# Kernel tuning notes

Measured on AMD Instinct MI355X. Metric: run time of the kernel, lower is better.

## Reference

```python
import jax, jax.numpy as jnp
import numpy as np

H = 2  # attention heads (n_heads)


def _time_enc(t, tw, tb):
    # TGN TimeEncode: cos(t * w + b); t [...,] -> [..., T]
    return jnp.cos(t[..., None] * tw + tb)


def _level0(nodes, node_features, memory_tab):
    # memory[src] + node_features[src]
    return memory_tab[nodes] + node_features[nodes]


def _aggregate(l, src_feat, src_te, neigh, ete, efeat, mask,
               Wq, bq, Wk, bk, Wv, bv, Wo, bo, fc1_w, fc1_b, fc2_w, fc2_b):
    # Temporal graph attention (TGN TemporalAttentionLayer) with padding mask.
    N, K, _ = neigh.shape
    Dq = Wq.shape[-1]
    dh = Dq // H
    q_in = jnp.concatenate([src_feat[:, None, :], src_te], axis=-1)   # [N,1,Dq]
    k_in = jnp.concatenate([neigh, ete, efeat], axis=-1)              # [N,K,Dk]
    q = (q_in @ Wq[l] + bq[l]).reshape(N, 1, H, dh)
    k = (k_in @ Wk[l] + bk[l]).reshape(N, K, H, dh)
    v = (k_in @ Wv[l] + bv[l]).reshape(N, K, H, dh)
    scores = jnp.einsum('nqhd,nkhd->nhqk', q, k) / jnp.sqrt(jnp.asarray(dh, q.dtype))
    all_masked = mask.all(axis=-1)                                    # [N]
    # TGN trick: un-mask column 0 for fully-masked rows, zero output later
    eff_mask = mask & ~(all_masked[:, None] & (jnp.arange(K) == 0))
    scores = jnp.where(eff_mask[:, None, None, :], -1e9, scores)
    attn = jax.nn.softmax(scores, axis=-1)
    o = jnp.einsum('nhqk,nkhd->nqhd', attn, v).reshape(N, Dq)
    o = o @ Wo[l] + bo[l]
    o = jnp.where(all_masked[:, None], 0.0, o)
    # MergeLayer: fc2(relu(fc1(cat[attn_out, src_feat])))
    h = jax.nn.relu(jnp.concatenate([o, src_feat], axis=-1) @ fc1_w[l] + fc1_b[l])
    return h @ fc2_w[l] + fc2_b[l]


def setup_inputs() -> dict:
    key = jax.random.key(0)
    ks = jax.random.split(key, 24)
    B, K, Nn, Ne, D, T = 2048, 20, 1_000_000, 1_000_000, 128, 128
    Dq, Dk = D + T, D + T + D
    inp = {}
    inp['node_features'] = jax.random.normal(ks[0], (Nn, D), jnp.float32) * 0.1
    inp['edge_feat_table'] = jax.random.normal(ks[1], (Ne, D), jnp.float32) * 0.1
    inp['memory_tab'] = jax.random.normal(ks[2], (Nn, D), jnp.float32) * 0.1
    inp['timestamps'] = jax.random.uniform(ks[3], (B,), jnp.float32) * 100.0
    inp['etimes_src'] = jax.random.uniform(ks[4], (B, K), jnp.float32) * 100.0
    inp['etimes_nbr'] = jax.random.uniform(ks[5], (B * K, K), jnp.float32) * 100.0
    inp['tw'] = jax.random.normal(ks[6], (T,), jnp.float32)
    inp['tb'] = jax.random.normal(ks[7], (T,), jnp.float32)
    inp['Wq'] = jax.random.normal(ks[8], (2, Dq, Dq), jnp.float32) / np.sqrt(Dq)
    inp['bq'] = jnp.zeros((2, Dq), jnp.float32)
    inp['Wk'] = jax.random.normal(ks[9], (2, Dk, Dq), jnp.float32) / np.sqrt(Dk)
    inp['bk'] = jnp.zeros((2, Dq), jnp.float32)
    inp['Wv'] = jax.random.normal(ks[10], (2, Dk, Dq), jnp.float32) / np.sqrt(Dk)
    inp['bv'] = jnp.zeros((2, Dq), jnp.float32)
    inp['Wo'] = jax.random.normal(ks[11], (2, Dq, Dq), jnp.float32) / np.sqrt(Dq)
    inp['bo'] = jnp.zeros((2, Dq), jnp.float32)
    inp['fc1_w'] = jax.random.normal(ks[12], (2, Dq + D, D), jnp.float32) / np.sqrt(Dq + D)
    inp['fc1_b'] = jnp.zeros((2, D), jnp.float32)
    inp['fc2_w'] = jax.random.normal(ks[13], (2, D, D), jnp.float32) / np.sqrt(D)
    inp['fc2_b'] = jnp.zeros((2, D), jnp.float32)
    inp['source_nodes'] = jax.random.randint(ks[14], (B,), 0, Nn)
    inp['nbrs_src'] = jax.random.randint(ks[15], (B, K), 0, Nn)
    inp['eidx_src'] = jax.random.randint(ks[16], (B, K), 0, Ne)
    inp['nbrs_nbr'] = jax.random.randint(ks[17], (B * K, K), 0, Nn)
    inp['eidx_nbr'] = jax.random.randint(ks[18], (B * K, K), 0, Ne)
    return inp


def reference(node_features, edge_feat_table, memory_tab, timestamps,
              etimes_src, etimes_nbr, tw, tb,
              Wq, bq, Wk, bk, Wv, bv, Wo, bo, fc1_w, fc1_b, fc2_w, fc2_b,
              source_nodes, nbrs_src, eidx_src, nbrs_nbr, eidx_nbr):
    B, K = nbrs_src.shape
    D = node_features.shape[-1]
    params = (Wq, bq, Wk, bk, Wv, bv, Wo, bo, fc1_w, fc1_b, fc2_w, fc2_b)

    def layer1(nodes, ts, nbrs, eidx, etimes):
        # one temporal-attention hop (n_layers == 1 recursion level)
        src = _level0(nodes, node_features, memory_tab)                 # [N,D]
        neigh = _level0(nbrs.reshape(-1), node_features, memory_tab).reshape(*nbrs.shape, D)
        ete = _time_enc(ts[:, None] - etimes, tw, tb)                   # [N,K,T]
        src_te = _time_enc(jnp.zeros((nodes.shape[0], 1), ts.dtype), tw, tb)
        efeat = edge_feat_table[eidx]                                   # [N,K,De]
        mask = nbrs == 0
        return _aggregate(0, src, src_te, neigh, ete, efeat, mask, *params)

    # layer-1 embedding of sources (recursion uses same temporal neighbors)
    src_conv = layer1(source_nodes, timestamps, nbrs_src, eidx_src, etimes_src)  # [B,D]
    # layer-1 embedding of the sources' neighbors
    ts_rep = jnp.repeat(timestamps, K)                                  # [B*K]
    neigh_emb = layer1(nbrs_src.reshape(-1), ts_rep, nbrs_nbr, eidx_nbr, etimes_nbr)
    neigh_emb = neigh_emb.reshape(B, K, D)
    # layer-2 aggregation over the sources' neighbors
    ete = _time_enc(timestamps[:, None] - etimes_src, tw, tb)           # [B,K,T]
    src_te = _time_enc(jnp.zeros((B, 1), timestamps.dtype), tw, tb)
    efeat = edge_feat_table[eidx_src]
    mask = nbrs_src == 0
    return _aggregate(1, src_conv, src_te, neigh_emb, ete, efeat, mask, *params)
```

## Files before the change

### kernel.cpp

```cpp
#include <hip/hip_runtime.h>
#include <hip/hip_bf16.h>

#define NB   2048
#define KN   20
#define DF   128
#define DQ   256
#define DKI  384
#define NR1  43008
#define SCALE 0.08838834764831845f

typedef short s16x8 __attribute__((ext_vector_type(8)));
typedef short s16x4 __attribute__((ext_vector_type(4)));
typedef float f32x4 __attribute__((ext_vector_type(4)));

__device__ __hip_bfloat16 g_S   [(size_t)NR1*256];
__device__ __hip_bfloat16 g_QKH [(size_t)NR1*768];
__device__ __hip_bfloat16 g_CTX [(size_t)NR1*768];
__device__ __hip_bfloat16 g_Ob  [(size_t)NR1*256];
__device__ __hip_bfloat16 g_FC1A[(size_t)NR1*384];
__device__ __hip_bfloat16 g_Hb  [(size_t)NR1*128];
__device__ float          g_out1[(size_t)NR1*DF];
__device__ float          g_Wqk [2*256*768];
__device__ float          g_bqk [2*768];
__device__ unsigned char  g_allm[NR1];
__device__ __hip_bfloat16 g_Bqk[2*196608];
__device__ __hip_bfloat16 g_Bv [2*196608];
__device__ __hip_bfloat16 g_Bo [2*65536];
__device__ __hip_bfloat16 g_B1 [2*49152];
__device__ __hip_bfloat16 g_B2 [2*16384];

__device__ __forceinline__ short f2bf(float v) {
  union { __hip_bfloat16 h; short s; } u; u.h = __float2bfloat16(v); return u.s;
}
__device__ __forceinline__ float bf2f(__hip_bfloat16 h) {
  union { __hip_bfloat16 h2[2]; unsigned u; float f; } x;
  x.u = 0; x.h2[1] = h; return x.f;
}
__device__ __forceinline__ s16x4 pack4(float x, float y, float z, float w) {
  s16x4 o; o[0]=f2bf(x); o[1]=f2bf(y); o[2]=f2bf(z); o[3]=f2bf(w); return o;
}

__global__ __launch_bounds__(256)
void k_wqk(const float* __restrict__ Wq, const float* __restrict__ Wk,
           const float* __restrict__ bq) {
  int idx = blockIdx.x*256 + threadIdx.x;
  int L = idx / 196608, rem = idx % 196608;
  int n = rem >> 8, co = rem & 255;
  int h = n / 384, i = n - h*384;
  const float* wqp = Wq + (size_t)L*DQ*DQ  + (size_t)co*DQ + h*128;
  const float* wkp = Wk + (size_t)L*DKI*DQ + (size_t)i*DQ  + h*128;
  float acc = 0.f;
  #pragma unroll 4
  for (int c = 0; c < 128; ++c) acc += wqp[c]*wkp[c];
  g_Wqk[(size_t)(L*256 + co)*768 + n] = acc;
  if (co == 0) {
    const float* bqp = bq + L*DQ + h*128;
    float b = 0.f;
    for (int c = 0; c < 128; ++c) b += bqp[c]*wkp[c];
    g_bqk[L*768 + n] = b;
  }
}

__global__ __launch_bounds__(256)
void k_btile(const float* __restrict__ src, int ldsrc, int K, int N,
             __hip_bfloat16* __restrict__ dst, int blkdiag) {
  int slot = blockIdx.x*256 + threadIdx.x;
  if (slot >= (K*N)/8) return;
  int cl = slot & 15, t = slot >> 4;
  int kgn = K >> 3;
  int kg = t % kgn, nt = t / kgn;
  int n = nt*16 + cl;
  s16x8 o;
  #pragma unroll
  for (int e = 0; e < 8; ++e) {
    int k = kg*8 + e; float v;
    if (blkdiag) { int hk = k / 384; v = (hk == (n >> 7)) ? src[(size_t)(k - hk*384)*ldsrc + n] : 0.f; }
    else v = src[(size_t)k*ldsrc + n];
    o[e] = f2bf(v);
  }
  *(s16x8*)(dst + (size_t)slot*8) = o;
}

template<int L>
__global__ __launch_bounds__(256)
void k_prep(const float* __restrict__ nf, const float* __restrict__ mem,
            const float* __restrict__ tb,
            const int* __restrict__ srcn, const int* __restrict__ nbs) {
  const int tid = threadIdx.x;
  const int rl = tid >> 5, q = tid & 31, d0 = q*4;
  const int r = blockIdx.x*8 + rl;
  float ax, ay, az, aw;
  if (L == 0) {
    int node = (r < NB) ? srcn[r] : nbs[r - NB];
    float4 x = *(const float4*)(mem + (size_t)node*DF + d0);
    float4 y = *(const float4*)(nf  + (size_t)node*DF + d0);
    ax=x.x+y.x; ay=x.y+y.y; az=x.z+y.z; aw=x.w+y.w;
  } else {
    float4 x = *(const float4*)(g_out1 + (size_t)r*DF + d0);
    ax=x.x; ay=x.y; az=x.z; aw=x.w;
  }
  *(s16x4*)(g_S + (size_t)r*256 + d0) = pack4(ax, ay, az, aw);
  *(s16x4*)(g_S + (size_t)r*256 + 128 + d0) =
      pack4(cosf(tb[d0]), cosf(tb[d0+1]), cosf(tb[d0+2]), cosf(tb[d0+3]));
  *(s16x4*)(g_FC1A + (size_t)r*384 + 256 + d0) = pack4(ax, ay, az, aw);
}

template<int L>
__global__ __launch_bounds__(256)
void k_edge(const float* __restrict__ nf, const float* __restrict__ ef,
            const float* __restrict__ mem, const float* __restrict__ tsv,
            const float* __restrict__ ets, const float* __restrict__ etn,
            const float* __restrict__ tw,  const float* __restrict__ tb,
            const int* __restrict__ nbs, const int* __restrict__ eis,
            const int* __restrict__ nbn, const int* __restrict__ ein,
            const __hip_bfloat16* __restrict__ QKH,
            __hip_bfloat16* __restrict__ CTX)
{
  const int r = blockIdx.x, tid = threadIdx.x;
  const int lane = tid & 63, w = tid >> 6;

  __shared__ int   nd[KN], ei[KN];
  __shared__ float dts[KN];
  __shared__ float s_sh[2][KN];
  __shared__ float aw_sh[2][KN];
  __shared__ float ctxp[4][768];
  __shared__ unsigned mbits_sh;

  int raw_ = 1;
  if (tid < KN) {
    int nd_, ei_; float dt_;
    if (L == 0) {
      if (r < NB) { raw_ = nbs[r*KN+tid]; nd_ = raw_; ei_ = eis[r*KN+tid]; dt_ = tsv[r] - ets[r*KN+tid]; }
      else { int mm = (r-NB)*KN + tid; raw_ = nbn[mm]; nd_ = raw_; ei_ = ein[mm]; dt_ = tsv[(r-NB)/KN] - etn[mm]; }
    } else {
      raw_ = nbs[r*KN+tid]; nd_ = NB + r*KN + tid; ei_ = eis[r*KN+tid]; dt_ = tsv[r] - ets[r*KN+tid];
    }
    nd[tid] = nd_; ei[tid] = ei_; dts[tid] = dt_;
  }
  if (tid < 64) {
    unsigned long long bal = __ballot(tid < KN && raw_ == 0);
    if (tid == 0) {
      unsigned mb = (unsigned)(bal & 0xFFFFFull);
      mbits_sh = mb;
      g_allm[r] = (mb == 0xFFFFFu) ? 1 : 0;
    }
  }

  float q0[6], q1[6];
  #pragma unroll
  for (int j = 0; j < 6; ++j) {
    q0[j] = bf2f(QKH[(size_t)r*768 +       j*64 + lane]);
    q1[j] = bf2f(QKH[(size_t)r*768 + 384 + j*64 + lane]);
  }
  float twr0 = tw[lane],      twr1 = tw[64 + lane];
  float tbr0 = tb[lane],      tbr1 = tb[64 + lane];
  __syncthreads();

  float ve[5][6];
  #pragma unroll
  for (int e = 0; e < 5; ++e) {
    const int m = w*5 + e;
    const int nd_ = nd[m], ei_ = ei[m];
    const float dt_ = dts[m];
    float v0, v1;
    if (L == 0) {
      v0 = mem[(size_t)nd_*DF +      lane] + nf[(size_t)nd_*DF +      lane];
      v1 = mem[(size_t)nd_*DF + 64 + lane] + nf[(size_t)nd_*DF + 64 + lane];
    } else {
      v0 = g_out1[(size_t)nd_*DF +      lane];
      v1 = g_out1[(size_t)nd_*DF + 64 + lane];
    }
    float v2 = __cosf(dt_*twr0 + tbr0);
    float v3 = __cosf(dt_*twr1 + tbr1);
    float v4 = ef[(size_t)ei_*DF +      lane];
    float v5 = ef[(size_t)ei_*DF + 64 + lane];
    ve[e][0]=v0; ve[e][1]=v1; ve[e][2]=v2; ve[e][3]=v3; ve[e][4]=v4; ve[e][5]=v5;
    float p0 = v0*q0[0] + v1*q0[1] + v2*q0[2] + v3*q0[3] + v4*q0[4] + v5*q0[5];
    float p1 = v0*q1[0] + v1*q1[1] + v2*q1[2] + v3*q1[3] + v4*q1[4] + v5*q1[5];
    #pragma unroll
    for (int off = 1; off < 64; off <<= 1) {
      p0 += __shfl_xor(p0, off);
      p1 += __shfl_xor(p1, off);
    }
    if (lane == 0) { s_sh[0][m] = p0; s_sh[1][m] = p1; }
  }
  __syncthreads();

  if (tid < 64) {
    const int h = tid >> 5, mm = tid & 31;
    const unsigned mb = mbits_sh;
    float sc;
    if (mm < KN) sc = ((mb >> mm) & 1u) ? -1e9f : s_sh[h][mm] * SCALE;
    else         sc = -3.0e38f;
    float mx = sc;
    #pragma unroll
    for (int off = 1; off < 32; off <<= 1) mx = fmaxf(mx, __shfl_xor(mx, off));
    float ev = (mm < KN) ? __expf(sc - mx) : 0.f;
    float sum = ev;
    #pragma unroll
    for (int off = 1; off < 32; off <<= 1) sum += __shfl_xor(sum, off);
    if (mm < KN) aw_sh[h][mm] = ev / sum;
  }
  __syncthreads();

  {
    float c0[6] = {0,0,0,0,0,0}, c1[6] = {0,0,0,0,0,0};
    #pragma unroll
    for (int e = 0; e < 5; ++e) {
      const int m = w*5 + e;
      const float a0 = aw_sh[0][m], a1 = aw_sh[1][m];
      #pragma unroll
      for (int j = 0; j < 6; ++j) {
        c0[j] += a0 * ve[e][j];
        c1[j] += a1 * ve[e][j];
      }
    }
    #pragma unroll
    for (int j = 0; j < 6; ++j) {
      ctxp[w][      j*64 + lane] = c0[j];
      ctxp[w][384 + j*64 + lane] = c1[j];
    }
  }
  __syncthreads();

  #pragma unroll
  for (int it = 0; it < 3; ++it) {
    int o = it*256 + tid;
    float s = ctxp[0][o] + ctxp[1][o] + ctxp[2][o] + ctxp[3][o];
    CTX[(size_t)r*768 + o] = __float2bfloat16(s);
  }
}

template<int KT, bool F32OUT, bool RELU, bool MASK>
__global__ __launch_bounds__(256, 2)
void k_gemm(const __hip_bfloat16* __restrict__ A, int lda,
            const __hip_bfloat16* __restrict__ B, int kgtot, int nblk,
            void* __restrict__ Cout, int ldc,
            const float* __restrict__ bias,
            const unsigned char* __restrict__ mask)
{
  __shared__ __hip_bfloat16 As[2][128*40];
  __shared__ __hip_bfloat16 Bs[2][128*32];
  const int tid  = threadIdx.x;
  const int lane = tid & 63, wid = tid >> 6;
  const int wm = wid >> 1, wn = wid & 1;
  const int rl = lane & 15, kgs = lane >> 4;
  const int bm = blockIdx.x / nblk, bn = blockIdx.x % nblk;

  f32x4 acc[4][4];
  #pragma unroll
  for (int i = 0; i < 4; ++i)
    #pragma unroll
    for (int j = 0; j < 4; ++j) acc[i][j] = (f32x4){0.f,0.f,0.f,0.f};

  #define STAGE(T, BUF) {                                                      \
    _Pragma("unroll")                                                          \
    for (int i_ = 0; i_ < 2; ++i_) {                                           \
      int row_ = i_*64 + (tid >> 2), kc_ = (tid & 3)*8;                        \
      s16x8 v_ = *(const s16x8*)(A + (size_t)(bm*128 + row_)*lda + (T)*32 + kc_); \
      *(s16x8*)(&As[BUF][row_*40 + kc_]) = v_;                                 \
    }                                                                          \
    _Pragma("unroll")                                                          \
    for (int i_ = 0; i_ < 2; ++i_) {                                           \
      int slot_ = i_*256 + tid;                                                \
      int nt_ = slot_ >> 6, kg_ = (slot_ >> 4) & 3, cl_ = slot_ & 15;          \
      s16x8 w_ = *(const s16x8*)(B + ((size_t)(bn*8 + nt_)*kgtot + (T)*4 + kg_)*128 + cl_*8); \
      *(s16x8*)(&Bs[BUF][slot_*8]) = w_;                                       \
    } }

  STAGE(0, 0);
  __syncthreads();
  int buf = 0;
  for (int t = 0; t < KT; ++t) {
    if (t < KT-1) STAGE(t+1, buf ^ 1);
    s16x8 af[4], bfm[4];
    #pragma unroll
    for (int mtl = 0; mtl < 4; ++mtl)
      af[mtl] = *(const s16x8*)(&As[buf][(wm*64 + mtl*16 + rl)*40 + kgs*8]);
    #pragma unroll
    for (int ntl = 0; ntl < 4; ++ntl)
      bfm[ntl] = *(const s16x8*)(&Bs[buf][((wn*4 + ntl)*4 + kgs)*128 + rl*8]);
    #pragma unroll
    for (int mtl = 0; mtl < 4; ++mtl)
      #pragma unroll
      for (int ntl = 0; ntl < 4; ++ntl)
        acc[mtl][ntl] = __builtin_amdgcn_mfma_f32_16x16x32_bf16(af[mtl], bfm[ntl], acc[mtl][ntl], 0, 0, 0);
    __syncthreads();
    buf ^= 1;
  }
  #undef STAGE

  #pragma unroll
  for (int mtl = 0; mtl < 4; ++mtl) {
    #pragma unroll
    for (int ntl = 0; ntl < 4; ++ntl) {
      int gcol = bn*128 + wn*64 + ntl*16 + rl;
      float bb = bias ? bias[gcol] : 0.f;
      #pragma unroll
      for (int rg = 0; rg < 4; ++rg) {
        int grow = bm*128 + wm*64 + mtl*16 + kgs*4 + rg;
        float v = acc[mtl][ntl][rg] + bb;
        if (RELU) v = fmaxf(v, 0.f);
        if (MASK) { if (mask[grow]) v = 0.f; }
        if (F32OUT) ((float*)Cout)[(size_t)grow*ldc + gcol] = v;
        else ((__hip_bfloat16*)Cout)[(size_t)grow*ldc + gcol] = __float2bfloat16(v);
      }
    }
  }
}

extern "C" void kernel_launch(void* const* d_in, const int* in_sizes, int n_in,
                              void* d_out, int out_size, void* d_ws, size_t ws_size,
                              hipStream_t stream) {
  (void)in_sizes; (void)n_in; (void)out_size; (void)ws_size; (void)d_ws;
  const float* nf   = (const float*)d_in[0];
  const float* ef   = (const float*)d_in[1];
  const float* mem  = (const float*)d_in[2];
  const float* tsv  = (const float*)d_in[3];
  const float* ets  = (const float*)d_in[4];
  const float* etn  = (const float*)d_in[5];
  const float* tw   = (const float*)d_in[6];
  const float* tb   = (const float*)d_in[7];
  const float* Wq   = (const float*)d_in[8];
  const float* bq   = (const float*)d_in[9];
  const float* Wk   = (const float*)d_in[10];
  const float* bv   = (const float*)d_in[13];
  const float* Wv   = (const float*)d_in[12];
  const float* Wo   = (const float*)d_in[14];
  const float* bo   = (const float*)d_in[15];
  const float* f1w  = (const float*)d_in[16];
  const float* f1b  = (const float*)d_in[17];
  const float* f2w  = (const float*)d_in[18];
  const float* f2b  = (const float*)d_in[19];
  const int* srcn   = (const int*)d_in[20];
  const int* nbs    = (const int*)d_in[21];
  const int* eis    = (const int*)d_in[22];
  const int* nbn    = (const int*)d_in[23];
  const int* ein    = (const int*)d_in[24];
  float* out = (float*)d_out;

  __hip_bfloat16 *S, *QKH, *CTX, *Ob, *FC1A, *Hb, *Bqk, *Bv, *Bo, *B1, *B2;
  float *Wqkf, *bqkf, *out1f;
  unsigned char* allm;
  hipGetSymbolAddress((void**)&S,    HIP_SYMBOL(g_S));
  hipGetSymbolAddress((void**)&QKH,  HIP_SYMBOL(g_QKH));
  hipGetSymbolAddress((void**)&CTX,  HIP_SYMBOL(g_CTX));
  hipGetSymbolAddress((void**)&Ob,   HIP_SYMBOL(g_Ob));
  hipGetSymbolAddress((void**)&FC1A, HIP_SYMBOL(g_FC1A));
  hipGetSymbolAddress((void**)&Hb,   HIP_SYMBOL(g_Hb));
  hipGetSymbolAddress((void**)&Bqk,  HIP_SYMBOL(g_Bqk));
  hipGetSymbolAddress((void**)&Bv,   HIP_SYMBOL(g_Bv));
  hipGetSymbolAddress((void**)&Bo,   HIP_SYMBOL(g_Bo));
  hipGetSymbolAddress((void**)&B1,   HIP_SYMBOL(g_B1));
  hipGetSymbolAddress((void**)&B2,   HIP_SYMBOL(g_B2));
  hipGetSymbolAddress((void**)&Wqkf, HIP_SYMBOL(g_Wqk));
  hipGetSymbolAddress((void**)&bqkf, HIP_SYMBOL(g_bqk));
  hipGetSymbolAddress((void**)&out1f,HIP_SYMBOL(g_out1));
  hipGetSymbolAddress((void**)&allm, HIP_SYMBOL(g_allm));

  hipLaunchKernelGGL(k_wqk, dim3(1536), dim3(256), 0, stream, Wq, Wk, bq);
  for (int L = 0; L < 2; ++L) {
    hipLaunchKernelGGL(k_btile, dim3(96),  dim3(256), 0, stream, Wqkf + (size_t)L*256*768, 768, 256, 768, Bqk + (size_t)L*196608, 0);
    hipLaunchKernelGGL(k_btile, dim3(96),  dim3(256), 0, stream, Wv + (size_t)L*DKI*DQ,    256, 768, 256, Bv  + (size_t)L*196608, 1);
    hipLaunchKernelGGL(k_btile, dim3(32),  dim3(256), 0, stream, Wo + (size_t)L*DQ*DQ,     256, 256, 256, Bo  + (size_t)L*65536,  0);
    hipLaunchKernelGGL(k_btile, dim3(24),  dim3(256), 0, stream, f1w + (size_t)L*384*128,  128, 384, 128, B1  + (size_t)L*49152,  0);
    hipLaunchKernelGGL(k_btile, dim3(8),   dim3(256), 0, stream, f2w + (size_t)L*128*128,  128, 128, 128, B2  + (size_t)L*16384,  0);
  }

  {
    const int R = NR1, BMg = R/128;
    hipLaunchKernelGGL((k_prep<0>), dim3(R/8), dim3(256), 0, stream, nf, mem, tb, srcn, nbs);
    hipLaunchKernelGGL((k_gemm<8,false,false,false>), dim3(BMg*6), dim3(256), 0, stream,
        S, 256, Bqk, 32, 6, QKH, 768, bqkf, (const unsigned char*)nullptr);
    hipLaunchKernelGGL((k_edge<0>), dim3(R), dim3(256), 0, stream,
        nf, ef, mem, tsv, ets, etn, tw, tb, nbs, eis, nbn, ein, QKH, CTX);
    hipLaunchKernelGGL((k_gemm<24,false,false,false>), dim3(BMg*2), dim3(256), 0, stream,
        CTX, 768, Bv, 96, 2, Ob, 256, bv, (const unsigned char*)nullptr);
    hipLaunchKernelGGL((k_gemm<8,false,false,true>), dim3(BMg*2), dim3(256), 0, stream,
        Ob, 256, Bo, 32, 2, FC1A, 384, bo, allm);
    hipLaunchKernelGGL((k_gemm<12,false,true,false>), dim3(BMg), dim3(256), 0, stream,
        FC1A, 384, B1, 48, 1, Hb, 128, f1b, (const unsigned char*)nullptr);
    hipLaunchKernelGGL((k_gemm<4,true,false,false>), dim3(BMg), dim3(256), 0, stream,
        Hb, 128, B2, 16, 1, out1f, 128, f2b, (const unsigned char*)nullptr);
  }
  {
    const int R = NB, BMg = R/128;
    hipLaunchKernelGGL((k_prep<1>), dim3(R/8), dim3(256), 0, stream, nf, mem, tb, srcn, nbs);
    hipLaunchKernelGGL((k_gemm<8,false,false,false>), dim3(BMg*6), dim3(256), 0, stream,
        S, 256, Bqk + 196608, 32, 6, QKH, 768, bqkf + 768, (const unsigned char*)nullptr);
    hipLaunchKernelGGL((k_edge<1>), dim3(R), dim3(256), 0, stream,
        nf, ef, mem, tsv, ets, etn, tw, tb, nbs, eis, nbn, ein, QKH, CTX);
    hipLaunchKernelGGL((k_gemm<24,false,false,false>), dim3(BMg*2), dim3(256), 0, stream,
        CTX, 768, Bv + 196608, 96, 2, Ob, 256, bv + 256, (const unsigned char*)nullptr);
    hipLaunchKernelGGL((k_gemm<8,false,false,true>), dim3(BMg*2), dim3(256), 0, stream,
        Ob, 256, Bo + 65536, 32, 2, FC1A, 384, bo + 256, allm);
    hipLaunchKernelGGL((k_gemm<12,false,true,false>), dim3(BMg), dim3(256), 0, stream,
        FC1A, 384, B1 + 49152, 48, 1, Hb, 128, f1b + 128, (const unsigned char*)nullptr);
    hipLaunchKernelGGL((k_gemm<4,true,false,false>), dim3(BMg), dim3(256), 0, stream,
        Hb, 128, B2 + 16384, 16, 1, out, 128, f2b + 128, (const unsigned char*)nullptr);
  }
}
```

Before: 635.2 us.

## Split V projection per head and vectorize edge gathers with float2 loads

The block-diagonal V weight, which was padded with zeros to K=768, is replaced by two per-head GEMMs with K=384 each. This halves the MACs and the B-tile traffic of the context projection, at the cost of an extra launch. In the edge kernel, each lane now loads two adjacent elements with float2/packed-bf16 loads, and all gathers are issued before any compute to raise memory-level parallelism. k_edge also gets a launch-bounds occupancy hint, which may limit registers and cause spills.

After: 611.2 us. 1.04x faster.

```diff
diff --git a/kernel.cpp b/kernel.cpp
--- a/kernel.cpp
+++ b/kernel.cpp
@@ -24,7 +24,7 @@
 __device__ float          g_bqk [2*768];
 __device__ unsigned char  g_allm[NR1];
 __device__ __hip_bfloat16 g_Bqk[2*196608];
-__device__ __hip_bfloat16 g_Bv [2*196608];
+__device__ __hip_bfloat16 g_Bv [4*49152];
 __device__ __hip_bfloat16 g_Bo [2*65536];
 __device__ __hip_bfloat16 g_B1 [2*49152];
 __device__ __hip_bfloat16 g_B2 [2*16384];
@@ -32,9 +32,11 @@
 __device__ __forceinline__ short f2bf(float v) {
   union { __hip_bfloat16 h; short s; } u; u.h = __float2bfloat16(v); return u.s;
 }
-__device__ __forceinline__ float bf2f(__hip_bfloat16 h) {
-  union { __hip_bfloat16 h2[2]; unsigned u; float f; } x;
-  x.u = 0; x.h2[1] = h; return x.f;
+__device__ __forceinline__ float2 bfpair(unsigned u) {
+  union { unsigned u2; float f; } a, b;
+  a.u2 = u << 16;
+  b.u2 = u & 0xFFFF0000u;
+  float2 r; r.x = a.f; r.y = b.f; return r;
 }
 __device__ __forceinline__ s16x4 pack4(float x, float y, float z, float w) {
   s16x4 o; o[0]=f2bf(x); o[1]=f2bf(y); o[2]=f2bf(z); o[3]=f2bf(w); return o;
@@ -63,7 +65,7 @@
 
 __global__ __launch_bounds__(256)
 void k_btile(const float* __restrict__ src, int ldsrc, int K, int N,
-             __hip_bfloat16* __restrict__ dst, int blkdiag) {
+             __hip_bfloat16* __restrict__ dst) {
   int slot = blockIdx.x*256 + threadIdx.x;
   if (slot >= (K*N)/8) return;
   int cl = slot & 15, t = slot >> 4;
@@ -72,12 +74,7 @@
   int n = nt*16 + cl;
   s16x8 o;
   #pragma unroll
-  for (int e = 0; e < 8; ++e) {
-    int k = kg*8 + e; float v;
-    if (blkdiag) { int hk = k / 384; v = (hk == (n >> 7)) ? src[(size_t)(k - hk*384)*ldsrc + n] : 0.f; }
-    else v = src[(size_t)k*ldsrc + n];
-    o[e] = f2bf(v);
-  }
+  for (int e = 0; e < 8; ++e) o[e] = f2bf(src[(size_t)(kg*8 + e)*ldsrc + n]);
   *(s16x8*)(dst + (size_t)slot*8) = o;
 }
 
@@ -106,7 +103,7 @@
 }
 
 template<int L>
-__global__ __launch_bounds__(256)
+__global__ __launch_bounds__(256, 6)
 void k_edge(const float* __restrict__ nf, const float* __restrict__ ef,
             const float* __restrict__ mem, const float* __restrict__ tsv,
             const float* __restrict__ ets, const float* __restrict__ etn,
@@ -146,43 +143,54 @@
     }
   }
 
-  float q0[6], q1[6];
-  #pragma unroll
-  for (int j = 0; j < 6; ++j) {
-    q0[j] = bf2f(QKH[(size_t)r*768 +       j*64 + lane]);
-    q1[j] = bf2f(QKH[(size_t)r*768 + 384 + j*64 + lane]);
-  }
-  float twr0 = tw[lane],      twr1 = tw[64 + lane];
-  float tbr0 = tb[lane],      tbr1 = tb[64 + lane];
+  const __hip_bfloat16* Qr = QKH + (size_t)r*768;
+  float2 q0[3], q1[3];
+  #pragma unroll
+  for (int seg = 0; seg < 3; ++seg) {
+    q0[seg] = bfpair(*(const unsigned*)(Qr +       seg*128 + 2*lane));
+    q1[seg] = bfpair(*(const unsigned*)(Qr + 384 + seg*128 + 2*lane));
+  }
+  float2 twr = *(const float2*)(tw + 2*lane);
+  float2 tbr = *(const float2*)(tb + 2*lane);
   __syncthreads();
 
-  float ve[5][6];
+  int   nds[5], eir[5]; float dtr[5];
   #pragma unroll
   for (int e = 0; e < 5; ++e) {
-    const int m = w*5 + e;
-    const int nd_ = nd[m], ei_ = ei[m];
-    const float dt_ = dts[m];
-    float v0, v1;
+    int m = w*5 + e;
+    nds[e] = nd[m]; eir[e] = ei[m]; dtr[e] = dts[m];
+  }
+  float2 vm[5], vf[5], vef[5];
+  #pragma unroll
+  for (int e = 0; e < 5; ++e) {
     if (L == 0) {
-      v0 = mem[(size_t)nd_*DF +      lane] + nf[(size_t)nd_*DF +      lane];
-      v1 = mem[(size_t)nd_*DF + 64 + lane] + nf[(size_t)nd_*DF + 64 + lane];
+      vm[e] = *(const float2*)(mem + (size_t)nds[e]*DF + 2*lane);
+      vf[e] = *(const float2*)(nf  + (size_t)nds[e]*DF + 2*lane);
     } else {
-      v0 = g_out1[(size_t)nd_*DF +      lane];
-      v1 = g_out1[(size_t)nd_*DF + 64 + lane];
-    }
-    float v2 = __cosf(dt_*twr0 + tbr0);
-    float v3 = __cosf(dt_*twr1 + tbr1);
-    float v4 = ef[(size_t)ei_*DF +      lane];
-    float v5 = ef[(size_t)ei_*DF + 64 + lane];
-    ve[e][0]=v0; ve[e][1]=v1; ve[e][2]=v2; ve[e][3]=v3; ve[e][4]=v4; ve[e][5]=v5;
-    float p0 = v0*q0[0] + v1*q0[1] + v2*q0[2] + v3*q0[3] + v4*q0[4] + v5*q0[5];
-    float p1 = v0*q1[0] + v1*q1[1] + v2*q1[2] + v3*q1[3] + v4*q1[4] + v5*q1[5];
+      vm[e] = *(const float2*)(g_out1 + (size_t)nds[e]*DF + 2*lane);
+    }
+    vef[e] = *(const float2*)(ef + (size_t)eir[e]*DF + 2*lane);
+  }
+
+  float2 vn[5], vt[5];
+  #pragma unroll
+  for (int e = 0; e < 5; ++e) {
+    if (L == 0) { vn[e].x = vm[e].x + vf[e].x; vn[e].y = vm[e].y + vf[e].y; }
+    else        vn[e] = vm[e];
+    vt[e].x = __cosf(dtr[e]*twr.x + tbr.x);
+    vt[e].y = __cosf(dtr[e]*twr.y + tbr.y);
+    float p0 = vn[e].x*q0[0].x + vn[e].y*q0[0].y
+             + vt[e].x*q0[1].x + vt[e].y*q0[1].y
+             + vef[e].x*q0[2].x + vef[e].y*q0[2].y;
+    float p1 = vn[e].x*q1[0].x + vn[e].y*q1[0].y
+             + vt[e].x*q1[1].x + vt[e].y*q1[1].y
+             + vef[e].x*q1[2].x + vef[e].y*q1[2].y;
     #pragma unroll
     for (int off = 1; off < 64; off <<= 1) {
       p0 += __shfl_xor(p0, off);
       p1 += __shfl_xor(p1, off);
     }
-    if (lane == 0) { s_sh[0][m] = p0; s_sh[1][m] = p1; }
+    if (lane == 0) { s_sh[0][w*5+e] = p0; s_sh[1][w*5+e] = p1; }
   }
   __syncthreads();
 
@@ -204,22 +212,25 @@
   __syncthreads();
 
   {
-    float c0[6] = {0,0,0,0,0,0}, c1[6] = {0,0,0,0,0,0};
+    float2 c0n = {0,0}, c0t = {0,0}, c0e = {0,0};
+    float2 c1n = {0,0}, c1t = {0,0}, c1e = {0,0};
     #pragma unroll
     for (int e = 0; e < 5; ++e) {
       const int m = w*5 + e;
       const float a0 = aw_sh[0][m], a1 = aw_sh[1][m];
-      #pragma unroll
-      for (int j = 0; j < 6; ++j) {
-        c0[j] += a0 * ve[e][j];
-        c1[j] += a1 * ve[e][j];
-      }
-    }
-    #pragma unroll
-    for (int j = 0; j < 6; ++j) {
-      ctxp[w][      j*64 + lane] = c0[j];
-      ctxp[w][384 + j*64 + lane] = c1[j];
-    }
+      c0n.x += a0*vn[e].x;  c0n.y += a0*vn[e].y;
+      c0t.x += a0*vt[e].x;  c0t.y += a0*vt[e].y;
+      c0e.x += a0*vef[e].x; c0e.y += a0*vef[e].y;
+      c1n.x += a1*vn[e].x;  c1n.y += a1*vn[e].y;
+      c1t.x += a1*vt[e].x;  c1t.y += a1*vt[e].y;
+      c1e.x += a1*vef[e].x; c1e.y += a1*vef[e].y;
+    }
+    *(float2*)&ctxp[w][      2*lane] = c0n;
+    *(float2*)&ctxp[w][128 + 2*lane] = c0t;
+    *(float2*)&ctxp[w][256 + 2*lane] = c0e;
+    *(float2*)&ctxp[w][384 + 2*lane] = c1n;
+    *(float2*)&ctxp[w][512 + 2*lane] = c1t;
+    *(float2*)&ctxp[w][640 + 2*lane] = c1e;
   }
   __syncthreads();
 
@@ -360,11 +371,12 @@
 
   hipLaunchKernelGGL(k_wqk, dim3(1536), dim3(256), 0, stream, Wq, Wk, bq);
   for (int L = 0; L < 2; ++L) {
-    hipLaunchKernelGGL(k_btile, dim3(96),  dim3(256), 0, stream, Wqkf + (size_t)L*256*768, 768, 256, 768, Bqk + (size_t)L*196608, 0);
-    hipLaunchKernelGGL(k_btile, dim3(96),  dim3(256), 0, stream, Wv + (size_t)L*DKI*DQ,    256, 768, 256, Bv  + (size_t)L*196608, 1);
-    hipLaunchKernelGGL(k_btile, dim3(32),  dim3(256), 0, stream, Wo + (size_t)L*DQ*DQ,     256, 256, 256, Bo  + (size_t)L*65536,  0);
-    hipLaunchKernelGGL(k_btile, dim3(24),  dim3(256), 0, stream, f1w + (size_t)L*384*128,  128, 384, 128, B1  + (size_t)L*49152,  0);
-    hipLaunchKernelGGL(k_btile, dim3(8),   dim3(256), 0, stream, f2w + (size_t)L*128*128,  128, 128, 128, B2  + (size_t)L*16384,  0);
+    hipLaunchKernelGGL(k_btile, dim3(96), dim3(256), 0, stream, Wqkf + (size_t)L*256*768, 768, 256, 768, Bqk + (size_t)L*196608);
+    for (int h = 0; h < 2; ++h)
+      hipLaunchKernelGGL(k_btile, dim3(24), dim3(256), 0, stream, Wv + (size_t)L*DKI*DQ + h*128, 256, 384, 128, Bv + (size_t)(L*2+h)*49152);
+    hipLaunchKernelGGL(k_btile, dim3(32), dim3(256), 0, stream, Wo + (size_t)L*DQ*DQ,    256, 256, 256, Bo + (size_t)L*65536);
+    hipLaunchKernelGGL(k_btile, dim3(24), dim3(256), 0, stream, f1w + (size_t)L*384*128, 128, 384, 128, B1 + (size_t)L*49152);
+    hipLaunchKernelGGL(k_btile, dim3(8),  dim3(256), 0, stream, f2w + (size_t)L*128*128, 128, 128, 128, B2 + (size_t)L*16384);
   }
 
   {
@@ -374,8 +386,9 @@
         S, 256, Bqk, 32, 6, QKH, 768, bqkf, (const unsigned char*)nullptr);
     hipLaunchKernelGGL((k_edge<0>), dim3(R), dim3(256), 0, stream,
         nf, ef, mem, tsv, ets, etn, tw, tb, nbs, eis, nbn, ein, QKH, CTX);
-    hipLaunchKernelGGL((k_gemm<24,false,false,false>), dim3(BMg*2), dim3(256), 0, stream,
-        CTX, 768, Bv, 96, 2, Ob, 256, bv, (const unsigned char*)nullptr);
+    for (int h = 0; h < 2; ++h)
+      hipLaunchKernelGGL((k_gemm<12,false,false,false>), dim3(BMg), dim3(256), 0, stream,
+          CTX + h*384, 768, Bv + (size_t)h*49152, 48, 1, Ob + h*128, 256, bv + h*128, (const unsigned char*)nullptr);
     hipLaunchKernelGGL((k_gemm<8,false,false,true>), dim3(BMg*2), dim3(256), 0, stream,
         Ob, 256, Bo, 32, 2, FC1A, 384, bo, allm);
     hipLaunchKernelGGL((k_gemm<12,false,true,false>), dim3(BMg), dim3(256), 0, stream,
@@ -390,8 +403,9 @@
         S, 256, Bqk + 196608, 32, 6, QKH, 768, bqkf + 768, (const unsigned char*)nullptr);
     hipLaunchKernelGGL((k_edge<1>), dim3(R), dim3(256), 0, stream,
         nf, ef, mem, tsv, ets, etn, tw, tb, nbs, eis, nbn, ein, QKH, CTX);
-    hipLaunchKernelGGL((k_gemm<24,false,false,false>), dim3(BMg*2), dim3(256), 0, stream,
-        CTX, 768, Bv + 196608, 96, 2, Ob, 256, bv + 256, (const unsigned char*)nullptr);
+    for (int h = 0; h < 2; ++h)
+      hipLaunchKernelGGL((k_gemm<12,false,false,false>), dim3(BMg), dim3(256), 0, stream,
+          CTX + h*384, 768, Bv + (size_t)(2+h)*49152, 48, 1, Ob + h*128, 256, bv + 256 + h*128, (const unsigned char*)nullptr);
     hipLaunchKernelGGL((k_gemm<8,false,false,true>), dim3(BMg*2), dim3(256), 0, stream,
         Ob, 256, Bo + 65536, 32, 2, FC1A, 384, bo + 256, allm);
     hipLaunchKernelGGL((k_gemm<12,false,true,false>), dim3(BMg), dim3(256), 0, stream,
```
